# Kernel optimization log

Measured on AMD Instinct MI355X. Metric: run time of the kernel, lower is better.

## Reference

```python
import jax, jax.numpy as jnp
import numpy as np

EMBED = 512
HEADS = 8
HEAD_DIM = EMBED // HEADS


def setup_inputs() -> dict:
    key = jax.random.key(0)
    ks = jax.random.split(key, 7)
    N, Q, K = 8, 2048, 4096
    s = 1.0 / np.sqrt(EMBED)
    return {
        "x": jax.random.normal(ks[0], (N, Q, EMBED), dtype=jnp.float32),
        "y": jax.random.normal(ks[1], (N, K, EMBED), dtype=jnp.float32),
        "Wq": jax.random.normal(ks[2], (EMBED, EMBED), dtype=jnp.float32) * s,
        "Wk": jax.random.normal(ks[3], (EMBED, EMBED), dtype=jnp.float32) * s,
        "Wv": jax.random.normal(ks[4], (EMBED, EMBED), dtype=jnp.float32) * s,
        "Wo": jax.random.normal(ks[5], (EMBED, EMBED), dtype=jnp.float32) * s,
        "bo": jax.random.normal(ks[6], (EMBED,), dtype=jnp.float32) * 0.01,
    }


def reference(x, y, Wq, Wk, Wv, Wo, bo):
    N, Q, _ = x.shape
    K = y.shape[1]
    # torch Linear: out = in @ W.T
    queries = (x @ Wq.T).reshape(N, Q, HEADS, HEAD_DIM)
    keys = (y @ Wk.T).reshape(N, K, HEADS, HEAD_DIM)
    values = (y @ Wv.T).reshape(N, K, HEADS, HEAD_DIM)
    # NOTE: heads are SUMMED in the score einsum (head-collapsed attention)
    energy = jnp.einsum("nqhd,nkhd->nqk", queries, keys)  # [N,Q,K]
    attention = jax.nn.softmax(energy / jnp.sqrt(jnp.float32(EMBED)), axis=2)
    out = jnp.einsum("nqk,nkhd->nqhd", attention, values).reshape(N, Q, EMBED)
    return x + out @ Wo.T + bo
```

## Files before the change

### kernel.cpp

```cpp
#include <hip/hip_runtime.h>
#include <stdint.h>

typedef unsigned short u16;
typedef short bf16x8 __attribute__((ext_vector_type(8)));
typedef float f32x4 __attribute__((ext_vector_type(4)));
typedef u16 u16x8 __attribute__((ext_vector_type(8)));
typedef u16 u16x4v __attribute__((ext_vector_type(4)));
typedef uint32_t u32x2 __attribute__((ext_vector_type(2)));

#define EMBED 512
#define NBATCH 8
#define QLEN 2048
#define KLEN 4096

__device__ __forceinline__ u16 f2bf(float f) {
  uint32_t u = __builtin_bit_cast(uint32_t, f);
  u += 0x7fffu + ((u >> 16) & 1u);
  return (u16)(u >> 16);
}
__device__ __forceinline__ float bf2f(u16 b) {
  return __builtin_bit_cast(float, (uint32_t)b << 16);
}

__device__ __forceinline__ void gload_lds16(const void* g, void* lds) {
  __builtin_amdgcn_global_load_lds(
      (__attribute__((address_space(1))) void*)(uintptr_t)g,
      (__attribute__((address_space(3))) void*)(uint32_t)(uintptr_t)lds,
      16, 0, 0);
}

__global__ __launch_bounds__(256) void cvt_all_kernel(
    const float* __restrict__ x, const float* __restrict__ y,
    const float* __restrict__ wq, const float* __restrict__ wk,
    const float* __restrict__ wv, const float* __restrict__ wo,
    u16* __restrict__ dst) {
  const int64_t B0 = 2097152;
  const int64_t B1 = B0 + 4194304;
  const int64_t B2 = B1 + 65536;
  const int64_t B3 = B2 + 65536;
  const int64_t B4 = B3 + 65536;
  int64_t i = (int64_t)blockIdx.x * 256 + threadIdx.x;
  const float* src; int64_t off;
  if (i < B0)      { src = x;  off = 0;  }
  else if (i < B1) { src = y;  off = B0; }
  else if (i < B2) { src = wq; off = B1; }
  else if (i < B3) { src = wk; off = B2; }
  else if (i < B4) { src = wv; off = B3; }
  else             { src = wo; off = B4; }
  float4 f = ((const float4*)src)[i - off];
  u16x4v o = { f2bf(f.x), f2bf(f.y), f2bf(f.z), f2bf(f.w) };
  ((u16x4v*)dst)[i] = o;
}

constexpr int EPI_BF16 = 0;
constexpr int EPI_BF16_SCALE = 1;
constexpr int EPI_BF16_TRANS = 2;
constexpr int EPI_F32_RESID = 3;

template <int MODE>
__global__ __launch_bounds__(256, 2) void gemm_bt(
    const u16* __restrict__ A, const u16* __restrict__ B, void* __restrict__ Cv,
    int M, int N, int K,
    int64_t aBatch, int64_t bBatch, int64_t cBatch,
    float scale, const float* __restrict__ xres, const float* __restrict__ bias,
    u16* __restrict__ Vt) {
  __shared__ __align__(16) u16 As[128 * 64];
  __shared__ __align__(16) u16 Bs[128 * 64];

  const int tid = threadIdx.x;
  const int wave = tid >> 6;
  const int lane = tid & 63;
  const int bz = blockIdx.z;
  const int row0 = blockIdx.x * 128;
  const int col0 = blockIdx.y * 128;
  const u16* Ab = A + (int64_t)bz * aBatch;
  const u16* Bb = B + (int64_t)bz * bBatch;

  const int srow = wave * 32 + (lane >> 3);
  const int scol = (lane & 7) * 8;
  const u16* aSrc = Ab + (int64_t)(row0 + srow) * K + scol;
  const u16* bSrc = Bb + (int64_t)(col0 + srow) * K + scol;

  const int wm = (wave >> 1) * 64;
  const int wn = (wave & 1) * 64;
  const int fr = lane & 15;
  const int fq = lane >> 4;

  f32x4 acc[4][4];
#pragma unroll
  for (int mi = 0; mi < 4; ++mi)
#pragma unroll
    for (int ni = 0; ni < 4; ++ni) acc[mi][ni] = 0.0f;

  const int nkt = K >> 6;
  for (int kt = 0; kt < nkt; ++kt) {
    __syncthreads();
    const u16* aS = aSrc + kt * 64;
    const u16* bS = bSrc + kt * 64;
#pragma unroll
    for (int i = 0; i < 4; ++i) {
      gload_lds16(aS + (int64_t)(i * 8) * K, &As[(wave * 32 + i * 8) * 64]);
      gload_lds16(bS + (int64_t)(i * 8) * K, &Bs[(wave * 32 + i * 8) * 64]);
    }
    __syncthreads();
#pragma unroll
    for (int ks = 0; ks < 2; ++ks) {
      bf16x8 af[4], bfr[4];
#pragma unroll
      for (int mi = 0; mi < 4; ++mi)
        af[mi] = *(const bf16x8*)&As[(wm + mi * 16 + fr) * 64 + ks * 32 + fq * 8];
#pragma unroll
      for (int ni = 0; ni < 4; ++ni)
        bfr[ni] = *(const bf16x8*)&Bs[(wn + ni * 16 + fr) * 64 + ks * 32 + fq * 8];
#pragma unroll
      for (int mi = 0; mi < 4; ++mi)
#pragma unroll
        for (int ni = 0; ni < 4; ++ni)
          acc[mi][ni] = __builtin_amdgcn_mfma_f32_16x16x32_bf16(af[mi], bfr[ni],
                                                                acc[mi][ni], 0, 0, 0);
    }
  }

  if constexpr (MODE == EPI_BF16 || MODE == EPI_BF16_SCALE) {
    u16* C = (u16*)Cv + (int64_t)bz * cBatch;
#pragma unroll
    for (int mi = 0; mi < 4; ++mi) {
      const int rowb = row0 + wm + mi * 16 + fq * 4;
#pragma unroll
      for (int ni = 0; ni < 4; ++ni) {
        const int col = col0 + wn + ni * 16 + fr;
#pragma unroll
        for (int r = 0; r < 4; ++r) {
          float v = acc[mi][ni][r];
          if constexpr (MODE == EPI_BF16_SCALE) v *= scale;
          C[(int64_t)(rowb + r) * N + col] = f2bf(v);
        }
      }
    }
  } else if constexpr (MODE == EPI_BF16_TRANS) {
#pragma unroll
    for (int mi = 0; mi < 4; ++mi) {
      const int rowb = row0 + wm + mi * 16 + fq * 4;
      const int nb = rowb >> 12;
      const int kk = rowb & 4095;
#pragma unroll
      for (int ni = 0; ni < 4; ++ni) {
        const int col = col0 + wn + ni * 16 + fr;
        u16x4v o = { f2bf(acc[mi][ni][0]), f2bf(acc[mi][ni][1]),
                     f2bf(acc[mi][ni][2]), f2bf(acc[mi][ni][3]) };
        *(u16x4v*)&Vt[((int64_t)nb * EMBED + col) * KLEN + kk] = o;
      }
    }
  } else {
    float* C = (float*)Cv;
#pragma unroll
    for (int mi = 0; mi < 4; ++mi) {
      const int rowb = row0 + wm + mi * 16 + fq * 4;
#pragma unroll
      for (int ni = 0; ni < 4; ++ni) {
        const int col = col0 + wn + ni * 16 + fr;
        const float bv = bias[col];
#pragma unroll
        for (int r = 0; r < 4; ++r) {
          const int64_t idx = (int64_t)(rowb + r) * N + col;
          C[idx] = acc[mi][ni][r] + xres[idx] + bv;
        }
      }
    }
  }
}

__global__ __launch_bounds__(256, 1) void attn_kernel(
    const u16* __restrict__ Qm, const u16* __restrict__ Km,
    const u16* __restrict__ Vt, u16* __restrict__ O) {
  __shared__ __align__(16) u16 Ks[2][32 * 512];
  __shared__ __align__(16) u16 Vs[2][512 * 32];
  __shared__ __align__(16) u16 Pls[2][4 * 512];
  __shared__ __align__(16) float Als[2][64];

  const int tid = threadIdx.x;
  const int w = tid >> 6;
  const int lane = tid & 63;
  const int fr = lane & 15, fq = lane >> 4;
  const int s7 = fr & 7;
  const int frk = fr & 6;
  const int nb = blockIdx.x & 7;
  const int qt = blockIdx.x >> 3;

  bf16x8 q[16];
  {
    const u16* Qb = Qm + ((int64_t)nb * QLEN + qt * 64 + w * 16 + fr) * EMBED + fq * 8;
#pragma unroll
    for (int kc = 0; kc < 16; ++kc) q[kc] = *(const bf16x8*)&Qb[kc * 32];
  }

  f32x4 o[32];
#pragma unroll
  for (int i = 0; i < 32; ++i) o[i] = 0.0f;
  float mrun = -1e30f, lrun = 0.0f;

  const u16* Kb = Km + (int64_t)nb * KLEN * EMBED;
  const u16* Vb = Vt + (int64_t)nb * (int64_t)EMBED * KLEN;

  const int vrow = lane >> 2;
  const int vcl = (lane & 3) ^ ((lane >> 3) & 3);
  const int vswz = ((fr >> 1) & 3);

  {
    const u16* srcK = Kb + (int64_t)(w * 8) * EMBED;
#pragma unroll
    for (int i = 0; i < 8; ++i)
      gload_lds16(srcK + (int64_t)i * EMBED + (lane ^ i) * 8, &Ks[0][(w * 8 + i) * 512]);
#pragma unroll
    for (int i = 0; i < 8; ++i) {
      const int row0 = w * 128 + i * 16;
      gload_lds16(Vb + (int64_t)(row0 + vrow) * KLEN + vcl * 8, &Vs[0][row0 * 32]);
    }
  }
  __syncthreads();

  const int NT = KLEN / 32;
  for (int t = 0; t < NT; ++t) {
    const int cur = t & 1;
    const int prv = cur ^ 1;

    bf16x8 pa[4], vb[8];
    f32x4 ra[4];
    if (t > 0) {
#pragma unroll
      for (int qg = 0; qg < 4; ++qg)
        pa[qg] = *(const bf16x8*)&Pls[prv][qg * 512 + fr * 32 + (((2 * fq) ^ frk) * 4)];
#pragma unroll
      for (int qg = 0; qg < 4; ++qg)
        ra[qg] = *(const f32x4*)&Als[prv][qg * 16 + fq * 4];
#pragma unroll
      for (int dt = 0; dt < 8; ++dt)
        vb[dt] = *(const bf16x8*)&Vs[prv][((w * 128 + dt * 16) + fr) * 32 +
                                          ((fq ^ vswz) * 8)];
      asm volatile("s_waitcnt lgkmcnt(0)" ::: "memory");
      __builtin_amdgcn_sched_barrier(0);
    }

    if (t + 1 < NT) {
      const u16* srcK = Kb + ((int64_t)(t + 1) * 32 + w * 8) * EMBED;
#pragma unroll
      for (int i = 0; i < 8; ++i)
        gload_lds16(srcK + (int64_t)i * EMBED + (lane ^ i) * 8,
                    &Ks[prv][(w * 8 + i) * 512]);
#pragma unroll
      for (int i = 0; i < 8; ++i) {
        const int row0 = w * 128 + i * 16;
        gload_lds16(Vb + (int64_t)(row0 + vrow) * KLEN + (t + 1) * 32 + vcl * 8,
                    &Vs[prv][row0 * 32]);
      }
    }

    const u16* Kc = Ks[cur];
    f32x4 s0 = 0.0f, s1 = 0.0f;
#pragma unroll
    for (int kc = 0; kc < 16; ++kc) {
      bf16x8 k0 = *(const bf16x8*)&Kc[(fr)*512 + (((kc * 4 + fq) ^ s7) * 8)];
      bf16x8 k1 = *(const bf16x8*)&Kc[(16 + fr) * 512 + (((kc * 4 + fq) ^ s7) * 8)];
      s0 = __builtin_amdgcn_mfma_f32_16x16x32_bf16(k0, q[kc], s0, 0, 0, 0);
      s1 = __builtin_amdgcn_mfma_f32_16x16x32_bf16(k1, q[kc], s1, 0, 0, 0);
    }

    if (t > 0) {
      int nz = 0;
#pragma unroll
      for (int qg = 0; qg < 4; ++qg)
#pragma unroll
        for (int r = 0; r < 4; ++r) nz |= (ra[qg][r] != 1.0f);
      if (nz) {
#pragma unroll
        for (int qg = 0; qg < 4; ++qg)
#pragma unroll
          for (int dt = 0; dt < 8; ++dt)
#pragma unroll
            for (int r = 0; r < 4; ++r) o[qg * 8 + dt][r] *= ra[qg][r];
      }
#pragma unroll
      for (int qg = 0; qg < 4; ++qg)
#pragma unroll
        for (int dt = 0; dt < 8; ++dt)
          o[qg * 8 + dt] = __builtin_amdgcn_mfma_f32_16x16x32_bf16(
              pa[qg], vb[dt], o[qg * 8 + dt], 0, 0, 0);
    }

    float mt = fmaxf(fmaxf(fmaxf(s0[0], s0[1]), fmaxf(s0[2], s0[3])),
                     fmaxf(fmaxf(s1[0], s1[1]), fmaxf(s1[2], s1[3])));
    mt = fmaxf(mt, __shfl_xor(mt, 16));
    mt = fmaxf(mt, __shfl_xor(mt, 32));
    float alpha = 1.0f;
    if (!__all(mt <= mrun + 8.0f)) {
      const float mn = fmaxf(mrun, mt);
      alpha = __expf(mrun - mn);
      lrun *= alpha;
      mrun = mn;
    }
    float p0[4], p1[4];
    float rs = 0.0f;
#pragma unroll
    for (int r = 0; r < 4; ++r) {
      p0[r] = __expf(s0[r] - mrun);
      p1[r] = __expf(s1[r] - mrun);
      rs += p0[r] + p1[r];
    }
    rs += __shfl_xor(rs, 16);
    rs += __shfl_xor(rs, 32);
    lrun += rs;

    const uint32_t lo0 = (uint32_t)f2bf(p0[0]) | ((uint32_t)f2bf(p0[1]) << 16);
    const uint32_t lo1 = (uint32_t)f2bf(p0[2]) | ((uint32_t)f2bf(p0[3]) << 16);
    const uint32_t hi0 = (uint32_t)f2bf(p1[0]) | ((uint32_t)f2bf(p1[1]) << 16);
    const uint32_t hi1 = (uint32_t)f2bf(p1[2]) | ((uint32_t)f2bf(p1[3]) << 16);
    {
      u32x2 wlo = {lo0, lo1}, whi = {hi0, hi1};
      *(u32x2*)&Pls[cur][w * 512 + fr * 32 + ((fq ^ frk) * 4)] = wlo;
      *(u32x2*)&Pls[cur][w * 512 + fr * 32 + (((4 + fq) ^ frk) * 4)] = whi;
    }
    if (fq == 0) Als[cur][w * 16 + fr] = alpha;

    __syncthreads();
  }

  {
    const int prv = (NT - 1) & 1;
    bf16x8 pa[4], vb[8];
    f32x4 ra[4];
#pragma unroll
    for (int qg = 0; qg < 4; ++qg)
      pa[qg] = *(const bf16x8*)&Pls[prv][qg * 512 + fr * 32 + (((2 * fq) ^ frk) * 4)];
#pragma unroll
    for (int qg = 0; qg < 4; ++qg)
      ra[qg] = *(const f32x4*)&Als[prv][qg * 16 + fq * 4];
#pragma unroll
    for (int dt = 0; dt < 8; ++dt)
      vb[dt] = *(const bf16x8*)&Vs[prv][((w * 128 + dt * 16) + fr) * 32 +
                                        ((fq ^ vswz) * 8)];
    int nz = 0;
#pragma unroll
    for (int qg = 0; qg < 4; ++qg)
#pragma unroll
      for (int r = 0; r < 4; ++r) nz |= (ra[qg][r] != 1.0f);
    if (nz) {
#pragma unroll
      for (int qg = 0; qg < 4; ++qg)
#pragma unroll
        for (int dt = 0; dt < 8; ++dt)
#pragma unroll
          for (int r = 0; r < 4; ++r) o[qg * 8 + dt][r] *= ra[qg][r];
    }
#pragma unroll
    for (int qg = 0; qg < 4; ++qg)
#pragma unroll
      for (int dt = 0; dt < 8; ++dt)
        o[qg * 8 + dt] = __builtin_amdgcn_mfma_f32_16x16x32_bf16(
            pa[qg], vb[dt], o[qg * 8 + dt], 0, 0, 0);
  }

  if (fq == 0) Als[0][w * 16 + fr] = lrun;
  __syncthreads();
  f32x4 li[4];
#pragma unroll
  for (int qg = 0; qg < 4; ++qg) {
    f32x4 lv = *(const f32x4*)&Als[0][qg * 16 + fq * 4];
#pragma unroll
    for (int r = 0; r < 4; ++r) li[qg][r] = 1.0f / lv[r];
  }
  u16* Ob = O + ((int64_t)nb * QLEN + qt * 64) * EMBED + w * 128;
#pragma unroll
  for (int qg = 0; qg < 4; ++qg)
#pragma unroll
    for (int dt = 0; dt < 8; ++dt)
#pragma unroll
      for (int r = 0; r < 4; ++r)
        Ob[(int64_t)(qg * 16 + fq * 4 + r) * EMBED + dt * 16 + fr] =
            f2bf(o[qg * 8 + dt][r] * li[qg][r]);
}

extern "C" void kernel_launch(void* const* d_in, const int* in_sizes, int n_in,
                              void* d_out, int out_size, void* d_ws, size_t ws_size,
                              hipStream_t stream) {
  const float* x  = (const float*)d_in[0];
  const float* y  = (const float*)d_in[1];
  const float* Wq = (const float*)d_in[2];
  const float* Wk = (const float*)d_in[3];
  const float* Wv = (const float*)d_in[4];
  const float* Wo = (const float*)d_in[5];
  const float* bo = (const float*)d_in[6];
  float* out = (float*)d_out;

  const int64_t nx = (int64_t)NBATCH * QLEN * EMBED;
  const int64_t ny = (int64_t)NBATCH * KLEN * EMBED;
  const int64_t nw = (int64_t)EMBED * EMBED;

  u16* w   = (u16*)d_ws;
  u16* xb  = w;
  u16* O   = w; w += nx;
  u16* yb  = w; w += ny;
  u16* Wqb = w; w += nw;
  u16* Wkb = w; w += nw;
  u16* Wvb = w; w += nw;
  u16* Wob = w; w += nw;
  u16* Qm  = w; w += nx;
  u16* Km  = w; w += ny;
  u16* Vt  = w; w += ny;

  cvt_all_kernel<<<25600, 256, 0, stream>>>(x, y, Wq, Wk, Wv, Wo, xb);

  const float scal = 0.04419417382415922f;
  gemm_bt<EPI_BF16_SCALE><<<dim3(128, 4, 1), 256, 0, stream>>>(
      xb, Wqb, Qm, 16384, EMBED, EMBED, 0, 0, 0, scal, nullptr, nullptr, nullptr);
  gemm_bt<EPI_BF16><<<dim3(256, 4, 1), 256, 0, stream>>>(
      yb, Wkb, Km, 32768, EMBED, EMBED, 0, 0, 0, 1.f, nullptr, nullptr, nullptr);
  gemm_bt<EPI_BF16_TRANS><<<dim3(256, 4, 1), 256, 0, stream>>>(
      yb, Wvb, nullptr, 32768, EMBED, EMBED, 0, 0, 0, 1.f, nullptr, nullptr, Vt);

  attn_kernel<<<NBATCH * 32, 256, 0, stream>>>(Qm, Km, Vt, O);

  gemm_bt<EPI_F32_RESID><<<dim3(128, 4, 1), 256, 0, stream>>>(
      O, Wob, out, 16384, EMBED, EMBED, 0, 0, 0, 1.f, x, bo, nullptr);
}
```

Measured before the change: 461.6 us.

## Load V fragments one tile early into registers and prioritize MFMA phases

V fragments for the current tile are now read from LDS right after the QK^T MFMAs and held in registers (vbH) for the next iteration's PV step. This removes the explicit lgkmcnt wait and sched barrier at the top of each iteration, so the LDS reads can overlap other work. The MFMA blocks are wrapped in s_setprio, and the rescale check becomes a per-quad-group wave vote. The cost is 8 more live bf16x8 registers per lane, which may raise register pressure and lower occupancy. A barrier is added before the final Als write to avoid a race.

After: 984.2 us. +113.2%, slower.

```diff
diff --git a/kernel.cpp b/kernel.cpp
--- a/kernel.cpp
+++ b/kernel.cpp
@@ -219,12 +219,14 @@
   }
   __syncthreads();
 
+  bf16x8 vbH[8];
   const int NT = KLEN / 32;
+
   for (int t = 0; t < NT; ++t) {
     const int cur = t & 1;
     const int prv = cur ^ 1;
 
-    bf16x8 pa[4], vb[8];
+    bf16x8 pa[4];
     f32x4 ra[4];
     if (t > 0) {
 #pragma unroll
@@ -233,12 +235,6 @@
 #pragma unroll
       for (int qg = 0; qg < 4; ++qg)
         ra[qg] = *(const f32x4*)&Als[prv][qg * 16 + fq * 4];
-#pragma unroll
-      for (int dt = 0; dt < 8; ++dt)
-        vb[dt] = *(const bf16x8*)&Vs[prv][((w * 128 + dt * 16) + fr) * 32 +
-                                          ((fq ^ vswz) * 8)];
-      asm volatile("s_waitcnt lgkmcnt(0)" ::: "memory");
-      __builtin_amdgcn_sched_barrier(0);
     }
 
     if (t + 1 < NT) {
@@ -257,6 +253,7 @@
 
     const u16* Kc = Ks[cur];
     f32x4 s0 = 0.0f, s1 = 0.0f;
+    __builtin_amdgcn_s_setprio(1);
 #pragma unroll
     for (int kc = 0; kc < 16; ++kc) {
       bf16x8 k0 = *(const bf16x8*)&Kc[(fr)*512 + (((kc * 4 + fq) ^ s7) * 8)];
@@ -264,28 +261,36 @@
       s0 = __builtin_amdgcn_mfma_f32_16x16x32_bf16(k0, q[kc], s0, 0, 0, 0);
       s1 = __builtin_amdgcn_mfma_f32_16x16x32_bf16(k1, q[kc], s1, 0, 0, 0);
     }
+    __builtin_amdgcn_s_setprio(0);
+
+    bf16x8 vbN[8];
+    const u16* Vc = Vs[cur];
+#pragma unroll
+    for (int dt = 0; dt < 8; ++dt)
+      vbN[dt] = *(const bf16x8*)&Vc[((w * 128 + dt * 16) + fr) * 32 + ((fq ^ vswz) * 8)];
 
     if (t > 0) {
-      int nz = 0;
-#pragma unroll
-      for (int qg = 0; qg < 4; ++qg)
-#pragma unroll
-        for (int r = 0; r < 4; ++r) nz |= (ra[qg][r] != 1.0f);
-      if (nz) {
-#pragma unroll
-        for (int qg = 0; qg < 4; ++qg)
+#pragma unroll
+      for (int qg = 0; qg < 4; ++qg) {
+        if (__any(ra[qg][0] != 1.0f || ra[qg][1] != 1.0f ||
+                  ra[qg][2] != 1.0f || ra[qg][3] != 1.0f)) {
 #pragma unroll
           for (int dt = 0; dt < 8; ++dt)
 #pragma unroll
             for (int r = 0; r < 4; ++r) o[qg * 8 + dt][r] *= ra[qg][r];
-      }
+        }
+      }
+      __builtin_amdgcn_s_setprio(1);
 #pragma unroll
       for (int qg = 0; qg < 4; ++qg)
 #pragma unroll
         for (int dt = 0; dt < 8; ++dt)
           o[qg * 8 + dt] = __builtin_amdgcn_mfma_f32_16x16x32_bf16(
-              pa[qg], vb[dt], o[qg * 8 + dt], 0, 0, 0);
-    }
+              pa[qg], vbH[dt], o[qg * 8 + dt], 0, 0, 0);
+      __builtin_amdgcn_s_setprio(0);
+    }
+#pragma unroll
+    for (int dt = 0; dt < 8; ++dt) vbH[dt] = vbN[dt];
 
     float mt = fmaxf(fmaxf(fmaxf(s0[0], s0[1]), fmaxf(s0[2], s0[3])),
                      fmaxf(fmaxf(s1[0], s1[1]), fmaxf(s1[2], s1[3])));
@@ -325,40 +330,33 @@
   }
 
   {
-    const int prv = (NT - 1) & 1;
-    bf16x8 pa[4], vb[8];
+    bf16x8 pa[4];
     f32x4 ra[4];
 #pragma unroll
     for (int qg = 0; qg < 4; ++qg)
-      pa[qg] = *(const bf16x8*)&Pls[prv][qg * 512 + fr * 32 + (((2 * fq) ^ frk) * 4)];
+      pa[qg] = *(const bf16x8*)&Pls[1][qg * 512 + fr * 32 + (((2 * fq) ^ frk) * 4)];
 #pragma unroll
     for (int qg = 0; qg < 4; ++qg)
-      ra[qg] = *(const f32x4*)&Als[prv][qg * 16 + fq * 4];
-#pragma unroll
-    for (int dt = 0; dt < 8; ++dt)
-      vb[dt] = *(const bf16x8*)&Vs[prv][((w * 128 + dt * 16) + fr) * 32 +
-                                        ((fq ^ vswz) * 8)];
-    int nz = 0;
-#pragma unroll
-    for (int qg = 0; qg < 4; ++qg)
-#pragma unroll
-      for (int r = 0; r < 4; ++r) nz |= (ra[qg][r] != 1.0f);
-    if (nz) {
-#pragma unroll
-      for (int qg = 0; qg < 4; ++qg)
+      ra[qg] = *(const f32x4*)&Als[1][qg * 16 + fq * 4];
+#pragma unroll
+    for (int qg = 0; qg < 4; ++qg) {
+      if (__any(ra[qg][0] != 1.0f || ra[qg][1] != 1.0f ||
+                ra[qg][2] != 1.0f || ra[qg][3] != 1.0f)) {
 #pragma unroll
         for (int dt = 0; dt < 8; ++dt)
 #pragma unroll
           for (int r = 0; r < 4; ++r) o[qg * 8 + dt][r] *= ra[qg][r];
+      }
     }
 #pragma unroll
     for (int qg = 0; qg < 4; ++qg)
 #pragma unroll
       for (int dt = 0; dt < 8; ++dt)
         o[qg * 8 + dt] = __builtin_amdgcn_mfma_f32_16x16x32_bf16(
-            pa[qg], vb[dt], o[qg * 8 + dt], 0, 0, 0);
-  }
-
+            pa[qg], vbH[dt], o[qg * 8 + dt], 0, 0, 0);
+  }
+
+  __syncthreads();
   if (fq == 0) Als[0][w * 16 + fr] = lrun;
   __syncthreads();
   f32x4 li[4];
```
